# Kernel optimization log

Measured on AMD Instinct MI355X. Metric: run time of the kernel, lower is better.

Reference implementation:

```python
import jax, jax.numpy as jnp
import numpy as np

V, D, H, O = 500000, 64, 64, 64
N0, N1, N2, K = 8192, 100000, 300000, 32


def setup_inputs() -> dict:
    key = jax.random.key(0)
    ks = jax.random.split(key, 8)
    return {
        "feats": jax.random.normal(ks[0], (V, D), dtype=jnp.float32),
        "W0": jax.random.normal(ks[1], (D, H), dtype=jnp.float32) / jnp.sqrt(jnp.float32(D)),
        "b0": jnp.zeros((H,), jnp.float32),
        "W1": jax.random.normal(ks[2], (H, O), dtype=jnp.float32) / jnp.sqrt(jnp.float32(H)),
        "b1": jnp.zeros((O,), jnp.float32),
        "neigh_idx0": jax.random.randint(ks[3], (N0, K), 0, N1),  # seed -> positions in 1-hop layer
        "neigh_idx1": jax.random.randint(ks[4], (N1, K), 0, N2),  # 1-hop -> positions in 2-hop layer
        "node_ids1": jax.random.randint(ks[5], (N1,), 0, V),      # 1-hop node ids into feature table
        "node_ids2": jax.random.randint(ks[6], (N2,), 0, V),      # 2-hop node ids into feature table
    }


def reference(feats, W0, b0, W1, b1, neigh_idx0, neigh_idx1, node_ids1, node_ids2):
    # Embedding lookups (self.features(...)) for hop-1 and hop-2 node layers.
    v1 = feats[node_ids1]                       # [N1, D]
    v2 = feats[node_ids2]                       # [N2, D]
    # Layer i=0, hop=1: mean over sampled neighbors (mask.mm == gather-mean),
    # then linear0 + relu (dropout in eval mode == identity).
    agg1 = jnp.mean(v2[neigh_idx1], axis=1)     # [N1, D]
    h1 = jax.nn.relu(agg1 @ W0 + b0)            # [N1, H]
    # Layer i=1, hop=0: aggregate hop-1 representations for seed nodes, linear1 + relu.
    agg0 = jnp.mean(h1[neigh_idx0], axis=1)     # [N0, H]
    out = jax.nn.relu(agg0 @ W1 + b1)           # [N0, O]
    return out
```

## Files before the change

kernel.cpp:

```cpp
#include <hip/hip_runtime.h>

typedef _Float16 h2_t __attribute__((ext_vector_type(2)));

static __device__ __forceinline__ unsigned short f2h_bits(float x) {
    return __builtin_bit_cast(unsigned short, (_Float16)x);
}
static __device__ __forceinline__ unsigned pack_h2(float x, float y) {
    h2_t v = {(_Float16)x, (_Float16)y};
    return __builtin_bit_cast(unsigned, v);
}
static __device__ __forceinline__ float dot2f(unsigned a, unsigned b, float c) {
#if __has_builtin(__builtin_amdgcn_fdot2)
    return __builtin_amdgcn_fdot2(__builtin_bit_cast(h2_t, a),
                                  __builtin_bit_cast(h2_t, b), c, false);
#else
    const h2_t ha = __builtin_bit_cast(h2_t, a), hb = __builtin_bit_cast(h2_t, b);
    return fmaf((float)ha[1], (float)hb[1], fmaf((float)ha[0], (float)hb[0], c));
#endif
}
static __device__ __forceinline__ h2_t shx_add(h2_t v, int m) {
    return v + __builtin_bit_cast(h2_t, __shfl_xor(__builtin_bit_cast(int, v), m, 64));
}

__global__ __launch_bounds__(256) void k_cast(
    const float* __restrict__ feats,
    const int*   __restrict__ nid2,
    unsigned short* __restrict__ feats2,
    int N2)
{
    const int lane = threadIdx.x & 63;
    const int sub  = lane >> 4;
    const int c4   = lane & 15;
    const int gwave = blockIdx.x * (blockDim.x >> 6) + (threadIdx.x >> 6);
    const int nwave = gridDim.x * (blockDim.x >> 6);

    for (int base = 8 * gwave; base < N2; base += 8 * nwave) {
        const int t0 = base + sub;
        const int t1 = base + 4 + sub;
        const bool v0 = (t0 < N2), v1 = (t1 < N2);
        const int n0 = v0 ? nid2[t0] : 0;
        const int n1 = v1 ? nid2[t1] : 0;
        const float4 a = ((const float4*)feats)[(size_t)n0 * 16 + c4];
        const float4 b = ((const float4*)feats)[(size_t)n1 * 16 + c4];
        ushort4 sa, sb;
        sa.x = f2h_bits(a.x); sa.y = f2h_bits(a.y);
        sa.z = f2h_bits(a.z); sa.w = f2h_bits(a.w);
        sb.x = f2h_bits(b.x); sb.y = f2h_bits(b.y);
        sb.z = f2h_bits(b.z); sb.w = f2h_bits(b.w);
        if (v0) ((ushort4*)feats2)[(size_t)t0 * 16 + c4] = sa;
        if (v1) ((ushort4*)feats2)[(size_t)t1 * 16 + c4] = sb;
    }
}

template <bool IND, typename TT>
__global__ __launch_bounds__(256) void k_hop1(
    const TT*    __restrict__ table,
    const float* __restrict__ W0,
    const float* __restrict__ b0,
    const int*   __restrict__ idx1,
    const int*   __restrict__ nid2,
    unsigned short* __restrict__ h1,
    int N1)
{
    const int lane = threadIdx.x & 63;
    const int sub  = lane >> 4;
    const int c4   = lane & 15;
    const int gwave = blockIdx.x * (blockDim.x >> 6) + (threadIdx.x >> 6);
    const int nwave = gridDim.x * (blockDim.x >> 6);

    unsigned w0p[32];
#pragma unroll
    for (int p = 0; p < 32; ++p)
        w0p[p] = pack_h2(W0[(2 * p) * 64 + lane] * 0.03125f,
                         (2 * p + 1 < 64 ? W0[(2 * p + 1) * 64 + lane] : 0.f) * 0.03125f);
    const float bias = b0[lane];

    const int4* iv = (const int4*)idx1;

    for (int base = 2 * gwave; base < N1; base += 2 * nwave) {
        const int r0 = base;
        const bool has_r1 = (base + 1 < N1);
        const int r1 = has_r1 ? base + 1 : base;

        const int4 qa0 = iv[(size_t)r0 * 8 + 2 * sub];
        const int4 qb0 = iv[(size_t)r0 * 8 + 2 * sub + 1];
        const int4 qa1 = iv[(size_t)r1 * 8 + 2 * sub];
        const int4 qb1 = iv[(size_t)r1 * 8 + 2 * sub + 1];
        int nk0[8] = {qa0.x, qa0.y, qa0.z, qa0.w, qb0.x, qb0.y, qb0.z, qb0.w};
        int nk1[8] = {qa1.x, qa1.y, qa1.z, qa1.w, qb1.x, qb1.y, qb1.z, qb1.w};
        if constexpr (IND) {
#pragma unroll
            for (int i = 0; i < 8; ++i) {
                nk0[i] = nid2[nk0[i]];
                nk1[i] = nid2[nk1[i]];
            }
        }

        unsigned pk00, pk01, pk10, pk11;
        if constexpr (!IND) {
            h2_t a00 = {0, 0}, a01 = {0, 0}, a10 = {0, 0}, a11 = {0, 0};
#pragma unroll
            for (int i = 0; i < 8; ++i) {
                const uint2 v0 = ((const uint2*)table)[(size_t)nk0[i] * 16 + c4];
                const uint2 v1 = ((const uint2*)table)[(size_t)nk1[i] * 16 + c4];
                a00 += __builtin_bit_cast(h2_t, v0.x);
                a01 += __builtin_bit_cast(h2_t, v0.y);
                a10 += __builtin_bit_cast(h2_t, v1.x);
                a11 += __builtin_bit_cast(h2_t, v1.y);
            }
            a00 = shx_add(a00, 16); a00 = shx_add(a00, 32);
            a01 = shx_add(a01, 16); a01 = shx_add(a01, 32);
            a10 = shx_add(a10, 16); a10 = shx_add(a10, 32);
            a11 = shx_add(a11, 16); a11 = shx_add(a11, 32);
            pk00 = __builtin_bit_cast(unsigned, a00);
            pk01 = __builtin_bit_cast(unsigned, a01);
            pk10 = __builtin_bit_cast(unsigned, a10);
            pk11 = __builtin_bit_cast(unsigned, a11);
        } else {
            float a0[4] = {0.f, 0.f, 0.f, 0.f};
            float a1[4] = {0.f, 0.f, 0.f, 0.f};
#pragma unroll
            for (int i = 0; i < 8; ++i) {
                const float4 v0 = ((const float4*)table)[(size_t)nk0[i] * 16 + c4];
                const float4 v1 = ((const float4*)table)[(size_t)nk1[i] * 16 + c4];
                a0[0] += v0.x; a0[1] += v0.y; a0[2] += v0.z; a0[3] += v0.w;
                a1[0] += v1.x; a1[1] += v1.y; a1[2] += v1.z; a1[3] += v1.w;
            }
#pragma unroll
            for (int c = 0; c < 4; ++c) {
                a0[c] += __shfl_xor(a0[c], 16, 64);
                a0[c] += __shfl_xor(a0[c], 32, 64);
                a1[c] += __shfl_xor(a1[c], 16, 64);
                a1[c] += __shfl_xor(a1[c], 32, 64);
            }
            pk00 = __builtin_bit_cast(unsigned, __builtin_amdgcn_cvt_pkrtz(a0[0], a0[1]));
            pk01 = __builtin_bit_cast(unsigned, __builtin_amdgcn_cvt_pkrtz(a0[2], a0[3]));
            pk10 = __builtin_bit_cast(unsigned, __builtin_amdgcn_cvt_pkrtz(a1[0], a1[1]));
            pk11 = __builtin_bit_cast(unsigned, __builtin_amdgcn_cvt_pkrtz(a1[2], a1[3]));
        }

        float h0 = bias, h1v = bias;
#pragma unroll
        for (int p = 0; p < 32; ++p) {
            const unsigned a0p = (unsigned)__builtin_amdgcn_readlane(
                (int)(p & 1 ? pk01 : pk00), p >> 1);
            const unsigned a1p = (unsigned)__builtin_amdgcn_readlane(
                (int)(p & 1 ? pk11 : pk10), p >> 1);
            h0  = dot2f(a0p, w0p[p], h0);
            h1v = dot2f(a1p, w0p[p], h1v);
        }
        h0  = fmaxf(h0, 0.f);
        h1v = fmaxf(h1v, 0.f);

        h1[(size_t)r0 * 64 + lane] = f2h_bits(h0);
        if (has_r1) h1[(size_t)r1 * 64 + lane] = f2h_bits(h1v);
    }
}

__global__ __launch_bounds__(256) void k_hop0(
    const unsigned short* __restrict__ h1,
    const float* __restrict__ W1,
    const float* __restrict__ b1,
    const int*   __restrict__ idx0,
    float*       __restrict__ out,
    int N0)
{
    const int lane = threadIdx.x & 63;
    const int sub  = lane >> 4;
    const int c4   = lane & 15;
    const int gwave = blockIdx.x * (blockDim.x >> 6) + (threadIdx.x >> 6);
    const int nwave = gridDim.x * (blockDim.x >> 6);

    unsigned w1p[32];
#pragma unroll
    for (int p = 0; p < 32; ++p)
        w1p[p] = pack_h2(W1[(2 * p) * 64 + lane] * 0.03125f,
                         (2 * p + 1 < 64 ? W1[(2 * p + 1) * 64 + lane] : 0.f) * 0.03125f);
    const float bias = b1[lane];

    const int4* iv = (const int4*)idx0;

    for (int base = 2 * gwave; base < N0; base += 2 * nwave) {
        const int r0 = base;
        const bool has_r1 = (base + 1 < N0);
        const int r1 = has_r1 ? base + 1 : base;

        const int4 qa0 = iv[(size_t)r0 * 8 + 2 * sub];
        const int4 qb0 = iv[(size_t)r0 * 8 + 2 * sub + 1];
        const int4 qa1 = iv[(size_t)r1 * 8 + 2 * sub];
        const int4 qb1 = iv[(size_t)r1 * 8 + 2 * sub + 1];
        const int jk0[8] = {qa0.x, qa0.y, qa0.z, qa0.w, qb0.x, qb0.y, qb0.z, qb0.w};
        const int jk1[8] = {qa1.x, qa1.y, qa1.z, qa1.w, qb1.x, qb1.y, qb1.z, qb1.w};

        h2_t a00 = {0, 0}, a01 = {0, 0}, a10 = {0, 0}, a11 = {0, 0};
#pragma unroll
        for (int i = 0; i < 8; ++i) {
            const uint2 v0 = ((const uint2*)h1)[(size_t)jk0[i] * 16 + c4];
            const uint2 v1 = ((const uint2*)h1)[(size_t)jk1[i] * 16 + c4];
            a00 += __builtin_bit_cast(h2_t, v0.x);
            a01 += __builtin_bit_cast(h2_t, v0.y);
            a10 += __builtin_bit_cast(h2_t, v1.x);
            a11 += __builtin_bit_cast(h2_t, v1.y);
        }
        a00 = shx_add(a00, 16); a00 = shx_add(a00, 32);
        a01 = shx_add(a01, 16); a01 = shx_add(a01, 32);
        a10 = shx_add(a10, 16); a10 = shx_add(a10, 32);
        a11 = shx_add(a11, 16); a11 = shx_add(a11, 32);
        const unsigned pk00 = __builtin_bit_cast(unsigned, a00);
        const unsigned pk01 = __builtin_bit_cast(unsigned, a01);
        const unsigned pk10 = __builtin_bit_cast(unsigned, a10);
        const unsigned pk11 = __builtin_bit_cast(unsigned, a11);

        float o0 = bias, o1 = bias;
#pragma unroll
        for (int p = 0; p < 32; ++p) {
            const unsigned a0p = (unsigned)__builtin_amdgcn_readlane(
                (int)(p & 1 ? pk01 : pk00), p >> 1);
            const unsigned a1p = (unsigned)__builtin_amdgcn_readlane(
                (int)(p & 1 ? pk11 : pk10), p >> 1);
            o0 = dot2f(a0p, w1p[p], o0);
            o1 = dot2f(a1p, w1p[p], o1);
        }
        out[(size_t)r0 * 64 + lane] = fmaxf(o0, 0.f);
        if (has_r1) out[(size_t)r1 * 64 + lane] = fmaxf(o1, 0.f);
    }
}

extern "C" void kernel_launch(void* const* d_in, const int* in_sizes, int n_in,
                              void* d_out, int out_size, void* d_ws, size_t ws_size,
                              hipStream_t stream) {
    const float* feats = (const float*)d_in[0];
    const float* W0    = (const float*)d_in[1];
    const float* b0    = (const float*)d_in[2];
    const float* W1    = (const float*)d_in[3];
    const float* b1    = (const float*)d_in[4];
    const int*   idx0  = (const int*)d_in[5];
    const int*   idx1  = (const int*)d_in[6];
    const int*   nid2  = (const int*)d_in[8];

    const int N0 = in_sizes[5] / 32;
    const int N1 = in_sizes[6] / 32;
    const int N2 = in_sizes[8];

    const size_t bytes_feats2 = (size_t)N2 * 64 * 2;
    const size_t bytes_h1     = (size_t)N1 * 64 * 2;

    if (ws_size >= bytes_feats2 + bytes_h1) {
        unsigned short* feats2 = (unsigned short*)d_ws;
        unsigned short* h1     = (unsigned short*)((char*)d_ws + bytes_feats2);
        k_cast<<<2048, 256, 0, stream>>>(feats, nid2, feats2, N2);
        k_hop1<false, unsigned short><<<2048, 256, 0, stream>>>(
            feats2, W0, b0, idx1, nullptr, h1, N1);
        k_hop0<<<1024, 256, 0, stream>>>(h1, W1, b1, idx0, (float*)d_out, N0);
    } else {
        unsigned short* h1 = (unsigned short*)d_ws;
        k_hop1<true, float><<<2048, 256, 0, stream>>>(
            feats, W0, b0, idx1, nid2, h1, N1);
        k_hop0<<<1024, 256, 0, stream>>>(h1, W1, b1, idx0, (float*)d_out, N0);
    }
}
```

Before: 266.7 us.

## Prefetch next row's gathers in hop1, use 16B gathers and LDS weights

The cast kernel now handles four rows per lane group, so more independent loads are in flight. The hop1 f16 kernel and the hop0 kernel gather with 16-byte loads, so each half-wave handles one output row. They keep the packed weights in shared memory instead of 32 registers and add a launch-bounds occupancy hint. Hop1 also software-pipelines the next iteration's neighbor gathers while the current row is reduced and multiplied. This targets gather latency and register pressure, at the cost of LDS reads inside the dot loop and extra prefetch registers.

```diff
diff --git a/kernel.cpp b/kernel.cpp
--- a/kernel.cpp
+++ b/kernel.cpp
@@ -34,27 +34,119 @@
     const int gwave = blockIdx.x * (blockDim.x >> 6) + (threadIdx.x >> 6);
     const int nwave = gridDim.x * (blockDim.x >> 6);
 
-    for (int base = 8 * gwave; base < N2; base += 8 * nwave) {
-        const int t0 = base + sub;
-        const int t1 = base + 4 + sub;
-        const bool v0 = (t0 < N2), v1 = (t1 < N2);
-        const int n0 = v0 ? nid2[t0] : 0;
-        const int n1 = v1 ? nid2[t1] : 0;
-        const float4 a = ((const float4*)feats)[(size_t)n0 * 16 + c4];
-        const float4 b = ((const float4*)feats)[(size_t)n1 * 16 + c4];
-        ushort4 sa, sb;
-        sa.x = f2h_bits(a.x); sa.y = f2h_bits(a.y);
-        sa.z = f2h_bits(a.z); sa.w = f2h_bits(a.w);
-        sb.x = f2h_bits(b.x); sb.y = f2h_bits(b.y);
-        sb.z = f2h_bits(b.z); sb.w = f2h_bits(b.w);
-        if (v0) ((ushort4*)feats2)[(size_t)t0 * 16 + c4] = sa;
-        if (v1) ((ushort4*)feats2)[(size_t)t1 * 16 + c4] = sb;
-    }
-}
-
-template <bool IND, typename TT>
-__global__ __launch_bounds__(256) void k_hop1(
-    const TT*    __restrict__ table,
+    for (int base = 16 * gwave; base < N2; base += 16 * nwave) {
+        int t[4]; bool vv[4]; int n[4];
+#pragma unroll
+        for (int s = 0; s < 4; ++s) {
+            t[s]  = base + 4 * s + sub;
+            vv[s] = t[s] < N2;
+            n[s]  = vv[s] ? nid2[t[s]] : 0;
+        }
+        float4 a[4];
+#pragma unroll
+        for (int s = 0; s < 4; ++s)
+            a[s] = ((const float4*)feats)[(size_t)n[s] * 16 + c4];
+#pragma unroll
+        for (int s = 0; s < 4; ++s) {
+            ushort4 sa;
+            sa.x = f2h_bits(a[s].x); sa.y = f2h_bits(a[s].y);
+            sa.z = f2h_bits(a[s].z); sa.w = f2h_bits(a[s].w);
+            if (vv[s]) ((ushort4*)feats2)[(size_t)t[s] * 16 + c4] = sa;
+        }
+    }
+}
+
+__global__ __launch_bounds__(256, 4) void k_hop1_f16(
+    const unsigned short* __restrict__ table,
+    const float* __restrict__ W0,
+    const float* __restrict__ b0,
+    const int*   __restrict__ idx1,
+    unsigned short* __restrict__ h1,
+    int N1)
+{
+    __shared__ unsigned wlds[32 * 64];
+    for (int e = threadIdx.x; e < 2048; e += 256) {
+        const int p = e >> 6, l = e & 63;
+        wlds[e] = pack_h2(W0[(2 * p) * 64 + l] * 0.03125f,
+                          W0[(2 * p + 1) * 64 + l] * 0.03125f);
+    }
+    __syncthreads();
+
+    const int lane = threadIdx.x & 63;
+    const int g4   = (lane >> 3) & 3;
+    const int hi   = lane >> 5;
+    const int c8   = lane & 7;
+    const float bias = b0[lane];
+    const int gwave = blockIdx.x * (blockDim.x >> 6) + (threadIdx.x >> 6);
+    const int nwave = gridDim.x * (blockDim.x >> 6);
+
+    const int4*  iv = (const int4*)idx1;
+    const uint4* tp = (const uint4*)table;
+
+    int base = 2 * gwave;
+    if (base >= N1) return;
+
+    uint4 v[8];
+    {
+        const int rr = (base + 1 < N1) ? base + hi : base;
+        const int4 qa = iv[(size_t)rr * 8 + 2 * g4];
+        const int4 qb = iv[(size_t)rr * 8 + 2 * g4 + 1];
+        const int nk[8] = {qa.x, qa.y, qa.z, qa.w, qb.x, qb.y, qb.z, qb.w};
+#pragma unroll
+        for (int i = 0; i < 8; ++i)
+            v[i] = tp[(size_t)nk[i] * 8 + c8];
+    }
+
+    for (;;) {
+        const int nxt = base + 2 * nwave;
+        const bool more = nxt < N1;
+        uint4 w[8];
+        if (more) {
+            const int rr = (nxt + 1 < N1) ? nxt + hi : nxt;
+            const int4 qa = iv[(size_t)rr * 8 + 2 * g4];
+            const int4 qb = iv[(size_t)rr * 8 + 2 * g4 + 1];
+            const int nk[8] = {qa.x, qa.y, qa.z, qa.w, qb.x, qb.y, qb.z, qb.w};
+#pragma unroll
+            for (int i = 0; i < 8; ++i)
+                w[i] = tp[(size_t)nk[i] * 8 + c8];
+        }
+
+        h2_t acc[4] = {h2_t{0, 0}, h2_t{0, 0}, h2_t{0, 0}, h2_t{0, 0}};
+#pragma unroll
+        for (int i = 0; i < 8; ++i) {
+            acc[0] += __builtin_bit_cast(h2_t, v[i].x);
+            acc[1] += __builtin_bit_cast(h2_t, v[i].y);
+            acc[2] += __builtin_bit_cast(h2_t, v[i].z);
+            acc[3] += __builtin_bit_cast(h2_t, v[i].w);
+        }
+#pragma unroll
+        for (int j = 0; j < 4; ++j) {
+            acc[j] = shx_add(acc[j], 8);
+            acc[j] = shx_add(acc[j], 16);
+        }
+        float h0a = bias, h0b = 0.f, h1a = bias, h1b = 0.f;
+#pragma unroll
+        for (int p = 0; p < 32; ++p) {
+            const unsigned wp = wlds[p * 64 + lane];
+            const int av = __builtin_bit_cast(int, acc[p & 3]);
+            const unsigned a0 = (unsigned)__builtin_amdgcn_readlane(av, p >> 2);
+            const unsigned a1 = (unsigned)__builtin_amdgcn_readlane(av, 32 + (p >> 2));
+            if (p & 1) { h0b = dot2f(a0, wp, h0b); h1b = dot2f(a1, wp, h1b); }
+            else       { h0a = dot2f(a0, wp, h0a); h1a = dot2f(a1, wp, h1a); }
+        }
+        h1[(size_t)base * 64 + lane] = f2h_bits(fmaxf(h0a + h0b, 0.f));
+        if (base + 1 < N1)
+            h1[(size_t)(base + 1) * 64 + lane] = f2h_bits(fmaxf(h1a + h1b, 0.f));
+
+        if (!more) break;
+#pragma unroll
+        for (int i = 0; i < 8; ++i) v[i] = w[i];
+        base = nxt;
+    }
+}
+
+__global__ __launch_bounds__(256) void k_hop1_f32(
+    const float* __restrict__ table,
     const float* __restrict__ W0,
     const float* __restrict__ b0,
     const int*   __restrict__ idx1,
@@ -72,72 +164,43 @@
 #pragma unroll
     for (int p = 0; p < 32; ++p)
         w0p[p] = pack_h2(W0[(2 * p) * 64 + lane] * 0.03125f,
-                         (2 * p + 1 < 64 ? W0[(2 * p + 1) * 64 + lane] : 0.f) * 0.03125f);
+                         W0[(2 * p + 1) * 64 + lane] * 0.03125f);
     const float bias = b0[lane];
-
     const int4* iv = (const int4*)idx1;
 
     for (int base = 2 * gwave; base < N1; base += 2 * nwave) {
         const int r0 = base;
         const bool has_r1 = (base + 1 < N1);
         const int r1 = has_r1 ? base + 1 : base;
-
         const int4 qa0 = iv[(size_t)r0 * 8 + 2 * sub];
         const int4 qb0 = iv[(size_t)r0 * 8 + 2 * sub + 1];
         const int4 qa1 = iv[(size_t)r1 * 8 + 2 * sub];
         const int4 qb1 = iv[(size_t)r1 * 8 + 2 * sub + 1];
         int nk0[8] = {qa0.x, qa0.y, qa0.z, qa0.w, qb0.x, qb0.y, qb0.z, qb0.w};
         int nk1[8] = {qa1.x, qa1.y, qa1.z, qa1.w, qb1.x, qb1.y, qb1.z, qb1.w};
-        if constexpr (IND) {
-#pragma unroll
-            for (int i = 0; i < 8; ++i) {
-                nk0[i] = nid2[nk0[i]];
-                nk1[i] = nid2[nk1[i]];
-            }
-        }
-
-        unsigned pk00, pk01, pk10, pk11;
-        if constexpr (!IND) {
-            h2_t a00 = {0, 0}, a01 = {0, 0}, a10 = {0, 0}, a11 = {0, 0};
-#pragma unroll
-            for (int i = 0; i < 8; ++i) {
-                const uint2 v0 = ((const uint2*)table)[(size_t)nk0[i] * 16 + c4];
-                const uint2 v1 = ((const uint2*)table)[(size_t)nk1[i] * 16 + c4];
-                a00 += __builtin_bit_cast(h2_t, v0.x);
-                a01 += __builtin_bit_cast(h2_t, v0.y);
-                a10 += __builtin_bit_cast(h2_t, v1.x);
-                a11 += __builtin_bit_cast(h2_t, v1.y);
-            }
-            a00 = shx_add(a00, 16); a00 = shx_add(a00, 32);
-            a01 = shx_add(a01, 16); a01 = shx_add(a01, 32);
-            a10 = shx_add(a10, 16); a10 = shx_add(a10, 32);
-            a11 = shx_add(a11, 16); a11 = shx_add(a11, 32);
-            pk00 = __builtin_bit_cast(unsigned, a00);
-            pk01 = __builtin_bit_cast(unsigned, a01);
-            pk10 = __builtin_bit_cast(unsigned, a10);
-            pk11 = __builtin_bit_cast(unsigned, a11);
-        } else {
-            float a0[4] = {0.f, 0.f, 0.f, 0.f};
-            float a1[4] = {0.f, 0.f, 0.f, 0.f};
-#pragma unroll
-            for (int i = 0; i < 8; ++i) {
-                const float4 v0 = ((const float4*)table)[(size_t)nk0[i] * 16 + c4];
-                const float4 v1 = ((const float4*)table)[(size_t)nk1[i] * 16 + c4];
-                a0[0] += v0.x; a0[1] += v0.y; a0[2] += v0.z; a0[3] += v0.w;
-                a1[0] += v1.x; a1[1] += v1.y; a1[2] += v1.z; a1[3] += v1.w;
-            }
-#pragma unroll
-            for (int c = 0; c < 4; ++c) {
-                a0[c] += __shfl_xor(a0[c], 16, 64);
-                a0[c] += __shfl_xor(a0[c], 32, 64);
-                a1[c] += __shfl_xor(a1[c], 16, 64);
-                a1[c] += __shfl_xor(a1[c], 32, 64);
-            }
-            pk00 = __builtin_bit_cast(unsigned, __builtin_amdgcn_cvt_pkrtz(a0[0], a0[1]));
-            pk01 = __builtin_bit_cast(unsigned, __builtin_amdgcn_cvt_pkrtz(a0[2], a0[3]));
-            pk10 = __builtin_bit_cast(unsigned, __builtin_amdgcn_cvt_pkrtz(a1[0], a1[1]));
-            pk11 = __builtin_bit_cast(unsigned, __builtin_amdgcn_cvt_pkrtz(a1[2], a1[3]));
-        }
+#pragma unroll
+        for (int i = 0; i < 8; ++i) { nk0[i] = nid2[nk0[i]]; nk1[i] = nid2[nk1[i]]; }
+
+        float a0[4] = {0.f, 0.f, 0.f, 0.f};
+        float a1[4] = {0.f, 0.f, 0.f, 0.f};
+#pragma unroll
+        for (int i = 0; i < 8; ++i) {
+            const float4 v0 = ((const float4*)table)[(size_t)nk0[i] * 16 + c4];
+            const float4 v1 = ((const float4*)table)[(size_t)nk1[i] * 16 + c4];
+            a0[0] += v0.x; a0[1] += v0.y; a0[2] += v0.z; a0[3] += v0.w;
+            a1[0] += v1.x; a1[1] += v1.y; a1[2] += v1.z; a1[3] += v1.w;
+        }
+#pragma unroll
+        for (int c = 0; c < 4; ++c) {
+            a0[c] += __shfl_xor(a0[c], 16, 64);
+            a0[c] += __shfl_xor(a0[c], 32, 64);
+            a1[c] += __shfl_xor(a1[c], 16, 64);
+            a1[c] += __shfl_xor(a1[c], 32, 64);
+        }
+        const unsigned pk00 = __builtin_bit_cast(unsigned, __builtin_amdgcn_cvt_pkrtz(a0[0], a0[1]));
+        const unsigned pk01 = __builtin_bit_cast(unsigned, __builtin_amdgcn_cvt_pkrtz(a0[2], a0[3]));
+        const unsigned pk10 = __builtin_bit_cast(unsigned, __builtin_amdgcn_cvt_pkrtz(a1[0], a1[1]));
+        const unsigned pk11 = __builtin_bit_cast(unsigned, __builtin_amdgcn_cvt_pkrtz(a1[2], a1[3]));
 
         float h0 = bias, h1v = bias;
 #pragma unroll
@@ -149,80 +212,75 @@
             h0  = dot2f(a0p, w0p[p], h0);
             h1v = dot2f(a1p, w0p[p], h1v);
         }
-        h0  = fmaxf(h0, 0.f);
-        h1v = fmaxf(h1v, 0.f);
-
-        h1[(size_t)r0 * 64 + lane] = f2h_bits(h0);
-        if (has_r1) h1[(size_t)r1 * 64 + lane] = f2h_bits(h1v);
-    }
-}
-
-__global__ __launch_bounds__(256) void k_hop0(
-    const unsigned short* __restrict__ h1,
+        h1[(size_t)r0 * 64 + lane] = f2h_bits(fmaxf(h0, 0.f));
+        if (has_r1) h1[(size_t)r1 * 64 + lane] = f2h_bits(fmaxf(h1v, 0.f));
+    }
+}
+
+__global__ __launch_bounds__(256, 4) void k_hop0(
+    const unsigned short* __restrict__ h1t,
     const float* __restrict__ W1,
     const float* __restrict__ b1,
     const int*   __restrict__ idx0,
     float*       __restrict__ out,
     int N0)
 {
+    __shared__ unsigned wlds[32 * 64];
+    for (int e = threadIdx.x; e < 2048; e += 256) {
+        const int p = e >> 6, l = e & 63;
+        wlds[e] = pack_h2(W1[(2 * p) * 64 + l] * 0.03125f,
+                          W1[(2 * p + 1) * 64 + l] * 0.03125f);
+    }
+    __syncthreads();
+
     const int lane = threadIdx.x & 63;
-    const int sub  = lane >> 4;
-    const int c4   = lane & 15;
+    const int g4   = (lane >> 3) & 3;
+    const int hi   = lane >> 5;
+    const int c8   = lane & 7;
+    const float bias = b1[lane];
     const int gwave = blockIdx.x * (blockDim.x >> 6) + (threadIdx.x >> 6);
     const int nwave = gridDim.x * (blockDim.x >> 6);
 
-    unsigned w1p[32];
-#pragma unroll
-    for (int p = 0; p < 32; ++p)
-        w1p[p] = pack_h2(W1[(2 * p) * 64 + lane] * 0.03125f,
-                         (2 * p + 1 < 64 ? W1[(2 * p + 1) * 64 + lane] : 0.f) * 0.03125f);
-    const float bias = b1[lane];
-
-    const int4* iv = (const int4*)idx0;
+    const int4*  iv = (const int4*)idx0;
+    const uint4* tp = (const uint4*)h1t;
 
     for (int base = 2 * gwave; base < N0; base += 2 * nwave) {
-        const int r0 = base;
-        const bool has_r1 = (base + 1 < N0);
-        const int r1 = has_r1 ? base + 1 : base;
-
-        const int4 qa0 = iv[(size_t)r0 * 8 + 2 * sub];
-        const int4 qb0 = iv[(size_t)r0 * 8 + 2 * sub + 1];
-        const int4 qa1 = iv[(size_t)r1 * 8 + 2 * sub];
-        const int4 qb1 = iv[(size_t)r1 * 8 + 2 * sub + 1];
-        const int jk0[8] = {qa0.x, qa0.y, qa0.z, qa0.w, qb0.x, qb0.y, qb0.z, qb0.w};
-        const int jk1[8] = {qa1.x, qa1.y, qa1.z, qa1.w, qb1.x, qb1.y, qb1.z, qb1.w};
-
-        h2_t a00 = {0, 0}, a01 = {0, 0}, a10 = {0, 0}, a11 = {0, 0};
+        const int rr = (base + 1 < N0) ? base + hi : base;
+        const int4 qa = iv[(size_t)rr * 8 + 2 * g4];
+        const int4 qb = iv[(size_t)rr * 8 + 2 * g4 + 1];
+        const int nk[8] = {qa.x, qa.y, qa.z, qa.w, qb.x, qb.y, qb.z, qb.w};
+
+        uint4 v[8];
+#pragma unroll
+        for (int i = 0; i < 8; ++i)
+            v[i] = tp[(size_t)nk[i] * 8 + c8];
+
+        h2_t acc[4] = {h2_t{0, 0}, h2_t{0, 0}, h2_t{0, 0}, h2_t{0, 0}};
 #pragma unroll
         for (int i = 0; i < 8; ++i) {
-            const uint2 v0 = ((const uint2*)h1)[(size_t)jk0[i] * 16 + c4];
-            const uint2 v1 = ((const uint2*)h1)[(size_t)jk1[i] * 16 + c4];
-            a00 += __builtin_bit_cast(h2_t, v0.x);
-            a01 += __builtin_bit_cast(h2_t, v0.y);
-            a10 += __builtin_bit_cast(h2_t, v1.x);
-            a11 += __builtin_bit_cast(h2_t, v1.y);
-        }
-        a00 = shx_add(a00, 16); a00 = shx_add(a00, 32);
-        a01 = shx_add(a01, 16); a01 = shx_add(a01, 32);
-        a10 = shx_add(a10, 16); a10 = shx_add(a10, 32);
-        a11 = shx_add(a11, 16); a11 = shx_add(a11, 32);
-        const unsigned pk00 = __builtin_bit_cast(unsigned, a00);
-        const unsigned pk01 = __builtin_bit_cast(unsigned, a01);
-        const unsigned pk10 = __builtin_bit_cast(unsigned, a10);
-        const unsigned pk11 = __builtin_bit_cast(unsigned, a11);
-
-        float o0 = bias, o1 = bias;
+            acc[0] += __builtin_bit_cast(h2_t, v[i].x);
+            acc[1] += __builtin_bit_cast(h2_t, v[i].y);
+            acc[2] += __builtin_bit_cast(h2_t, v[i].z);
+            acc[3] += __builtin_bit_cast(h2_t, v[i].w);
+        }
+#pragma unroll
+        for (int j = 0; j < 4; ++j) {
+            acc[j] = shx_add(acc[j], 8);
+            acc[j] = shx_add(acc[j], 16);
+        }
+        float o0a = bias, o0b = 0.f, o1a = bias, o1b = 0.f;
 #pragma unroll
         for (int p = 0; p < 32; ++p) {
-            const unsigned a0p = (unsigned)__builtin_amdgcn_readlane(
-                (int)(p & 1 ? pk01 : pk00), p >> 1);
-            const unsigned a1p = (unsigned)__builtin_amdgcn_readlane(
-                (int)(p & 1 ? pk11 : pk10), p >> 1);
-            o0 = dot2f(a0p, w1p[p], o0);
-            o1 = dot2f(a1p, w1p[p], o1);
-        }
-        out[(size_t)r0 * 64 + lane] = fmaxf(o0, 0.f);
-        if (has_r1) out[(size_t)r1 * 64 + lane] = fmaxf(o1, 0.f);
+            const unsigned wp = wlds[p * 64 + lane];
+            const int av = __builtin_bit_cast(int, acc[p & 3]);
+            const unsigned a0 = (unsigned)__builtin_amdgcn_readlane(av, p >> 2);
+            const unsigned a1 = (unsigned)__builtin_amdgcn_readlane(av, 32 + (p >> 2));
+            if (p & 1) { o0b = dot2f(a0, wp, o0b); o1b = dot2f(a1, wp, o1b); }
+            else       { o0a = dot2f(a0, wp, o0a); o1a = dot2f(a1, wp, o1a); }
+        }
+        out[(size_t)base * 64 + lane] = fmaxf(o0a + o0b, 0.f);
+        if (base + 1 < N0)
+            out[(size_t)(base + 1) * 64 + lane] = fmaxf(o1a + o1b, 0.f);
     }
 }
 
@@ -249,13 +307,11 @@
         unsigned short* feats2 = (unsigned short*)d_ws;
         unsigned short* h1     = (unsigned short*)((char*)d_ws + bytes_feats2);
         k_cast<<<2048, 256, 0, stream>>>(feats, nid2, feats2, N2);
-        k_hop1<false, unsigned short><<<2048, 256, 0, stream>>>(
-            feats2, W0, b0, idx1, nullptr, h1, N1);
+        k_hop1_f16<<<2048, 256, 0, stream>>>(feats2, W0, b0, idx1, h1, N1);
         k_hop0<<<1024, 256, 0, stream>>>(h1, W1, b1, idx0, (float*)d_out, N0);
     } else {
         unsigned short* h1 = (unsigned short*)d_ws;
-        k_hop1<true, float><<<2048, 256, 0, stream>>>(
-            feats, W0, b0, idx1, nid2, h1, N1);
+        k_hop1_f32<<<2048, 256, 0, stream>>>(feats, W0, b0, idx1, nid2, h1, N1);
         k_hop0<<<1024, 256, 0, stream>>>(h1, W1, b1, idx0, (float*)d_out, N0);
     }
 }
```

Measured after the change: 264.4 us. Within noise of the previous version (-0.9%).
